# Kernel tuning notes

Measured on AMD Instinct MI355X. Metric: run time of the kernel, lower is better.

## Reference

```python
import jax, jax.numpy as jnp
import numpy as np

F = 32  # node channels (both convs)


def ecc_conv(x, src, dst, e, fgn_w, fgn_b, root, bias):
    """Edge-conditioned conv: per-edge kernel from edge feats, gather-matmul-scatter."""
    n_nodes = x.shape[0]
    n_edges = e.shape[0]
    f_in = x.shape[1]
    # filter-generating network: (E, S) -> (E, F_in*F_out) -> (E, F_in, F_out)
    kernels = (e @ fgn_w + fgn_b).reshape(n_edges, f_in, F)
    # gather source node feats, per-edge matmul
    messages = jnp.einsum('ef,efo->eo', x[src], kernels)
    # scatter-sum to target nodes
    agg = jax.ops.segment_sum(messages, dst, num_segments=n_nodes)
    return jax.nn.relu(agg + x @ root + bias)


def setup_inputs() -> dict:
    key = jax.random.key(0)
    ks = jax.random.split(key, 12)
    N, E, S = 50000, 200000, 16
    s = 0.05  # small init scale to keep activations bounded through relu
    return {
        'x': jax.random.normal(ks[0], (N, F), jnp.float32),
        'e': jax.random.normal(ks[1], (E, S), jnp.float32),
        'src': jax.random.randint(ks[2], (E,), 0, N, jnp.int32),
        'dst': jax.random.randint(ks[3], (E,), 0, N, jnp.int32),
        'fgn_w1': jax.random.normal(ks[4], (S, F * F), jnp.float32) * s,
        'fgn_b1': jnp.zeros((F * F,), jnp.float32),
        'root1': jax.random.normal(ks[5], (F, F), jnp.float32) * s,
        'bias1': jnp.zeros((F,), jnp.float32),
        'fgn_w2': jax.random.normal(ks[6], (S, F * F), jnp.float32) * s,
        'fgn_b2': jnp.zeros((F * F,), jnp.float32),
        'root2': jax.random.normal(ks[7], (F, F), jnp.float32) * s,
        'bias2': jnp.zeros((F,), jnp.float32),
        'dense_w': jax.random.normal(ks[8], (F, 1), jnp.float32) * s,
        'dense_b': jnp.zeros((1,), jnp.float32),
    }


def reference(x, e, src, dst, fgn_w1, fgn_b1, root1, bias1,
              fgn_w2, fgn_b2, root2, bias2, dense_w, dense_b):
    h = ecc_conv(x, src, dst, e, fgn_w1, fgn_b1, root1, bias1)
    h = ecc_conv(h, src, dst, e, fgn_w2, fgn_b2, root2, bias2)
    pooled = jnp.sum(h, axis=0)          # global sum pool over nodes -> (F,)
    return pooled @ dense_w + dense_b    # (1,)
```

## Files before the change

### kernel.cpp

```cpp
#include <hip/hip_runtime.h>
#include <hip/hip_bf16.h>

#define F 32
#define S 16
#define K2 544

typedef short v8s __attribute__((ext_vector_type(8)));
typedef float v4f __attribute__((ext_vector_type(4)));

__device__ __forceinline__ float bf_lo(unsigned u) { return __uint_as_float(u << 16); }
__device__ __forceinline__ float bf_hi(unsigned u) { return __uint_as_float(u & 0xffff0000u); }
__device__ __forceinline__ unsigned short f2bf(float f) {
    __hip_bfloat16 h = __float2bfloat16(f);
    return *(unsigned short*)&h;
}
__device__ __forceinline__ unsigned pack2(float a, float b) {
    return (unsigned)f2bf(a) | ((unsigned)f2bf(b) << 16);
}
static inline size_t align256(size_t b) { return (b + 255) & ~(size_t)255; }

__global__ __launch_bounds__(256) void convert_w2(
    const float* __restrict__ w1, const float* __restrict__ b1, const float* __restrict__ r1,
    const float* __restrict__ w2, const float* __restrict__ b2, const float* __restrict__ r2,
    unsigned short* __restrict__ W2t1, unsigned short* __restrict__ W2t2,
    unsigned short* __restrict__ Rt1,  unsigned short* __restrict__ Rt2)
{
    const int PER = 32 * K2 + 32 * 32;
    int tid = blockIdx.x * blockDim.x + threadIdx.x;
    if (tid >= 2 * PER) return;
    const int layer = tid / PER;
    const int rem   = tid % PER;
    const float* w = layer ? w2 : w1;
    const float* b = layer ? b2 : b1;
    const float* r = layer ? r2 : r1;
    if (rem < 32 * K2) {
        const int o = rem / K2;
        const int k = rem % K2;
        const int s = k >> 5, f = k & 31;
        const float v = (s < S) ? w[s * (F * F) + f * F + o] : b[f * F + o];
        (layer ? W2t2 : W2t1)[o * K2 + k] = f2bf(v);
    } else {
        const int q = rem - 32 * K2;
        const int o = q >> 5, f = q & 31;
        (layer ? Rt2 : Rt1)[o * F + f] = f2bf(r[f * F + o]);
    }
}

__global__ __launch_bounds__(256) void hist_kernel(
    const int* __restrict__ dst, int* __restrict__ cnt, int E)
{
    int e = blockIdx.x * blockDim.x + threadIdx.x;
    if (e < E) atomicAdd(&cnt[dst[e]], 1);
}

__global__ __launch_bounds__(256) void scan_partial(
    const int* __restrict__ cnt, int* __restrict__ partial, int N)
{
    const int i = blockIdx.x * 256 + threadIdx.x;
    int v = (i < N) ? cnt[i] : 0;
    #pragma unroll
    for (int off = 32; off > 0; off >>= 1) v += __shfl_down(v, off, 64);
    __shared__ int wsum[4];
    const int wave = threadIdx.x >> 6, lane = threadIdx.x & 63;
    if (lane == 0) wsum[wave] = v;
    __syncthreads();
    if (threadIdx.x == 0)
        partial[blockIdx.x] = wsum[0] + wsum[1] + wsum[2] + wsum[3];
}

__global__ void scan_top(int* __restrict__ partial, int M)
{
    const int t = threadIdx.x;
    int carry = 0;
    for (int base = 0; base < M; base += 64) {
        const int i = base + t;
        const int v0 = (i < M) ? partial[i] : 0;
        int v = v0;
        #pragma unroll
        for (int off = 1; off < 64; off <<= 1) {
            int u = __shfl_up(v, off, 64);
            if (t >= off) v += u;
        }
        if (i < M) partial[i] = carry + (v - v0);
        carry += __shfl(v, 63, 64);
    }
}

__global__ __launch_bounds__(256) void scan_final(
    const int* __restrict__ cnt, const int* __restrict__ partial,
    int* __restrict__ cursor, int* __restrict__ rowptr, int N)
{
    const int i = blockIdx.x * 256 + threadIdx.x;
    const int v0 = (i < N) ? cnt[i] : 0;
    int v = v0;
    const int wave = threadIdx.x >> 6, lane = threadIdx.x & 63;
    #pragma unroll
    for (int off = 1; off < 64; off <<= 1) {
        int u = __shfl_up(v, off, 64);
        if (lane >= off) v += u;
    }
    __shared__ int wsum[4];
    if (lane == 63) wsum[wave] = v;
    __syncthreads();
    int woff = 0;
    for (int ww = 0; ww < 4; ++ww) woff += (ww < wave) ? wsum[ww] : 0;
    if (i < N) {
        const int excl = partial[blockIdx.x] + woff + (v - v0);
        cursor[i] = excl;
        rowptr[i] = excl;
    }
}

__global__ __launch_bounds__(256) void scatter_kernel(
    const int* __restrict__ dst, int* __restrict__ cursor,
    int* __restrict__ perm, int E)
{
    int e = blockIdx.x * blockDim.x + threadIdx.x;
    if (e < E) {
        int p = atomicAdd(&cursor[dst[e]], 1);
        perm[p] = e;
    }
}

__global__ __launch_bounds__(256) void edge_msg(
    const float* __restrict__ xin,
    const float* __restrict__ ef,
    const int* __restrict__ src,
    const unsigned short* __restrict__ W2t,
    unsigned short* __restrict__ msg,
    int E)
{
    const int tid  = threadIdx.x;
    const int w    = tid >> 6;
    const int lane = tid & 63;
    const int lid  = lane & 15;
    const int quad = lane >> 4;

    const int tile = blockIdx.x * 4 + w;
    const int nTiles = (E + 15) >> 4;
    if (tile >= nTiles) return;

    const int  slot = tile * 16 + lid;
    const bool live = (slot < E);
    const int  e    = live ? slot : 0;
    const int  sn   = src[e];
    const float4* xp = (const float4*)(xin + (size_t)sn * F + quad * 8);
    const float4 xv0 = xp[0], xv1 = xp[1];
    const float4* efv = (const float4*)(ef + (size_t)e * S);
    const float4 c0 = efv[0], c1 = efv[1], c2 = efv[2], c3 = efv[3];

    v8s wa0[17], wa1[17];
    #pragma unroll
    for (int ck = 0; ck < 17; ++ck) {
        wa0[ck] = *(const v8s*)(W2t + (size_t)lid * K2        + ck * 32 + quad * 8);
        wa1[ck] = *(const v8s*)(W2t + (size_t)(16 + lid) * K2 + ck * 32 + quad * 8);
    }

    const float cs[S] = {c0.x, c0.y, c0.z, c0.w, c1.x, c1.y, c1.z, c1.w,
                         c2.x, c2.y, c2.z, c2.w, c3.x, c3.y, c3.z, c3.w};

    v4f acc0 = {0.f, 0.f, 0.f, 0.f};
    v4f acc1 = {0.f, 0.f, 0.f, 0.f};

    #pragma unroll
    for (int ck = 0; ck < S; ++ck) {
        const float sc = cs[ck];
        union { v8s s8; uint4 u4; } fr;
        fr.u4.x = pack2(sc * xv0.x, sc * xv0.y);
        fr.u4.y = pack2(sc * xv0.z, sc * xv0.w);
        fr.u4.z = pack2(sc * xv1.x, sc * xv1.y);
        fr.u4.w = pack2(sc * xv1.z, sc * xv1.w);
        acc0 = __builtin_amdgcn_mfma_f32_16x16x32_bf16(wa0[ck], fr.s8, acc0, 0, 0, 0);
        acc1 = __builtin_amdgcn_mfma_f32_16x16x32_bf16(wa1[ck], fr.s8, acc1, 0, 0, 0);
    }
    {
        union { v8s s8; uint4 u4; } fr;
        fr.u4.x = pack2(xv0.x, xv0.y);
        fr.u4.y = pack2(xv0.z, xv0.w);
        fr.u4.z = pack2(xv1.x, xv1.y);
        fr.u4.w = pack2(xv1.z, xv1.w);
        acc0 = __builtin_amdgcn_mfma_f32_16x16x32_bf16(wa0[16], fr.s8, acc0, 0, 0, 0);
        acc1 = __builtin_amdgcn_mfma_f32_16x16x32_bf16(wa1[16], fr.s8, acc1, 0, 0, 0);
    }

    if (live) {
        unsigned short* mp = msg + (size_t)slot * 32;
        uint2 p0, p1;
        p0.x = pack2(acc0[0], acc0[1]);
        p0.y = pack2(acc0[2], acc0[3]);
        p1.x = pack2(acc1[0], acc1[1]);
        p1.y = pack2(acc1[2], acc1[3]);
        *(uint2*)(mp + quad * 4)      = p0;
        *(uint2*)(mp + 16 + quad * 4) = p1;
    }
}

__global__ __launch_bounds__(256) void rootsum(
    const float* __restrict__ in,
    const unsigned short* __restrict__ msg,
    const int* __restrict__ perm,
    const int* __restrict__ rowptr,
    const int* __restrict__ cnt,
    const unsigned short* __restrict__ Rt,
    const float* __restrict__ bias,
    float* __restrict__ h,
    int N)
{
    __shared__ float acc[64 * 33];
    __shared__ unsigned short As[64 * F];
    const int tid  = threadIdx.x;
    const int n0   = blockIdx.x * 64;
    const int w    = tid >> 6;
    const int lane = tid & 63;
    const int lid  = lane & 15;
    const int quad = lane >> 4;

    {
        const int nl = tid >> 2;
        const int kq = tid & 3;
        int n = n0 + nl; if (n > N - 1) n = N - 1;
        const float4* xp = (const float4*)(in + (size_t)n * F + kq * 8);
        float4 v0 = xp[0], v1 = xp[1];
        uint4 pk;
        pk.x = pack2(v0.x, v0.y);
        pk.y = pack2(v0.z, v0.w);
        pk.z = pack2(v1.x, v1.y);
        pk.w = pack2(v1.z, v1.w);
        const int slot = ((nl >> 4) * 4 + kq) * 16 + (nl & 15);
        *(uint4*)(As + slot * 8) = pk;
    }

    {
        const int nl = tid >> 2;
        const int oq = tid & 3;
        const int n  = n0 + nl;
        float a[8];
        #pragma unroll
        for (int j = 0; j < 8; ++j) a[j] = 0.f;
        if (n < N) {
            const int k0 = rowptr[n];
            const int k1 = k0 + cnt[n];
            for (int k = k0; k < k1; ++k) {
                const int e = perm[k];
                const uint4 q = *(const uint4*)(msg + (size_t)e * 32 + oq * 8);
                a[0] += bf_lo(q.x); a[1] += bf_hi(q.x);
                a[2] += bf_lo(q.y); a[3] += bf_hi(q.y);
                a[4] += bf_lo(q.z); a[5] += bf_hi(q.z);
                a[6] += bf_lo(q.w); a[7] += bf_hi(q.w);
            }
        }
        float* ap = acc + nl * 33 + oq * 8;
        #pragma unroll
        for (int j = 0; j < 8; ++j) ap[j] = a[j];
    }
    __syncthreads();

    const int jt  = w & 1;
    const int ns0 = (w >> 1) * 2;
    const v8s rf = *(const v8s*)(Rt + (size_t)(jt * 16 + lid) * F + quad * 8);
    const int o0 = jt * 16 + quad * 4;
    const float4 bs = *(const float4*)(bias + o0);

    #pragma unroll
    for (int i = 0; i < 2; ++i) {
        const int ns = ns0 + i;
        const v8s af = *(const v8s*)(As + (((ns * 4 + quad) * 16) + lid) * 8);
        v4f d = {0.f, 0.f, 0.f, 0.f};
        d = __builtin_amdgcn_mfma_f32_16x16x32_bf16(rf, af, d, 0, 0, 0);
        const int n = n0 + ns * 16 + lid;
        if (n < N) {
            const float* ap = acc + (ns * 16 + lid) * 33 + o0;
            float4 hv;
            hv.x = fmaxf(d[0] + ap[0] + bs.x, 0.f);
            hv.y = fmaxf(d[1] + ap[1] + bs.y, 0.f);
            hv.z = fmaxf(d[2] + ap[2] + bs.z, 0.f);
            hv.w = fmaxf(d[3] + ap[3] + bs.w, 0.f);
            *(float4*)(h + (size_t)n * F + o0) = hv;
        }
    }
}

__global__ __launch_bounds__(256) void pool_kernel(
    const float* __restrict__ h, float* __restrict__ pooled, int N)
{
    const int c = threadIdx.x & (F - 1);
    const int rowsPerBlock = 256 / F;
    float p = 0.0f;
    for (int n = blockIdx.x * rowsPerBlock + (threadIdx.x >> 5);
         n < N; n += gridDim.x * rowsPerBlock)
        p += h[(size_t)n * F + c];
    __shared__ float red[256];
    red[threadIdx.x] = p;
    __syncthreads();
    for (int off = 128; off >= F; off >>= 1) {
        if (threadIdx.x < off) red[threadIdx.x] += red[threadIdx.x + off];
        __syncthreads();
    }
    if (threadIdx.x < F) atomicAdd(&pooled[threadIdx.x], red[threadIdx.x]);
}

__global__ void final_kernel(
    const float* __restrict__ pooled, const float* __restrict__ dw,
    const float* __restrict__ db, float* __restrict__ out)
{
    const int o = threadIdx.x;
    float v = (o < F) ? pooled[o] * dw[o] : 0.0f;
    #pragma unroll
    for (int off = 32; off > 0; off >>= 1) v += __shfl_down(v, off, 64);
    if (o == 0) out[0] = v + db[0];
}

__global__ __launch_bounds__(256, 2) void ecc_edge_slow(
    const float* __restrict__ x, const float* __restrict__ ef,
    const int* __restrict__ src, const int* __restrict__ dst,
    const float* __restrict__ W, const float* __restrict__ B,
    float* __restrict__ agg, int E)
{
    const int tid = blockIdx.x * blockDim.x + threadIdx.x;
    const bool live = (tid < E);
    const int e = live ? tid : (E - 1);
    const int sn = src[e], dn = dst[e];
    float xr[F];
    const float4* xp = (const float4*)(x + (size_t)sn * F);
    #pragma unroll
    for (int i = 0; i < F / 4; ++i) {
        float4 v = xp[i];
        xr[4*i+0] = v.x; xr[4*i+1] = v.y; xr[4*i+2] = v.z; xr[4*i+3] = v.w;
    }
    float acc[F];
    #pragma unroll
    for (int o = 0; o < F; ++o) acc[o] = 0.0f;
    const float* erow = ef + (size_t)e * S;
    for (int s = 0; s < S; ++s) {
        const float es = erow[s];
        const float* Ws = W + s * (F * F);
        #pragma unroll
        for (int f = 0; f < F; ++f) {
            const float z = es * xr[f];
            #pragma unroll
            for (int o = 0; o < F; ++o) acc[o] = fmaf(z, Ws[f * F + o], acc[o]);
        }
    }
    #pragma unroll
    for (int f = 0; f < F; ++f) {
        const float xf = xr[f];
        #pragma unroll
        for (int o = 0; o < F; ++o) acc[o] = fmaf(xf, B[f * F + o], acc[o]);
    }
    if (live) {
        float* ap = agg + (size_t)dn * F;
        #pragma unroll
        for (int o = 0; o < F; ++o) atomicAdd(ap + o, acc[o]);
    }
}

__global__ __launch_bounds__(256) void ecc_node_slow(
    const float* __restrict__ xin, const float* __restrict__ root,
    const float* __restrict__ bias, float* __restrict__ h, int N)
{
    int t = blockIdx.x * blockDim.x + threadIdx.x;
    if (t >= N * F) return;
    const int n = t >> 5, o = t & (F - 1);
    const float* xrow = xin + (size_t)n * F;
    float v = h[t] + bias[o];
    #pragma unroll
    for (int f = 0; f < F; ++f) v = fmaf(xrow[f], root[f * F + o], v);
    h[t] = fmaxf(v, 0.0f);
}

extern "C" void kernel_launch(void* const* d_in, const int* in_sizes, int n_in,
                              void* d_out, int out_size, void* d_ws, size_t ws_size,
                              hipStream_t stream) {
    const float* x      = (const float*)d_in[0];
    const float* efeat  = (const float*)d_in[1];
    const int*   src    = (const int*)d_in[2];
    const int*   dst    = (const int*)d_in[3];
    const float* fgn_w1 = (const float*)d_in[4];
    const float* fgn_b1 = (const float*)d_in[5];
    const float* root1  = (const float*)d_in[6];
    const float* bias1  = (const float*)d_in[7];
    const float* fgn_w2 = (const float*)d_in[8];
    const float* fgn_b2 = (const float*)d_in[9];
    const float* root2  = (const float*)d_in[10];
    const float* bias2  = (const float*)d_in[11];
    const float* dense_w = (const float*)d_in[12];
    const float* dense_b = (const float*)d_in[13];

    const int N = in_sizes[0] / F;
    const int E = in_sizes[2];

    const int gridP = (N + 255) / 256;

    const size_t pooledB = 256;
    const size_t cntB    = align256((size_t)N * 4);
    const size_t rowB    = align256((size_t)N * 4);
    const size_t curB    = align256((size_t)N * 4);
    const size_t partB   = align256((size_t)gridP * 4);
    const size_t permB   = align256((size_t)E * 4);
    const size_t msgB    = align256((size_t)E * 32 * 2);
    const size_t hB      = (size_t)N * F * 4;
    const size_t w2tB    = align256((size_t)32 * K2 * 2);
    const size_t rtB     = align256((size_t)32 * 32 * 2);

    const size_t offCnt  = pooledB;
    const size_t offRow  = offCnt + cntB;
    const size_t offCur  = offRow + rowB;
    const size_t offPart = offCur + curB;
    const size_t offPerm = offPart + partB;
    const size_t offMsg  = offPerm + permB;
    const size_t offH1   = offMsg + msgB;
    const size_t offH2   = offH1 + hB;
    const size_t offW1   = offH2 + hB;
    const size_t offW2   = offW1 + w2tB;
    const size_t offR1   = offW2 + w2tB;
    const size_t offR2   = offR1 + rtB;
    const size_t need    = offR2 + rtB;

    const int eB         = (E + 255) / 256;
    const int nodeBlocks = (N * F + 255) / 256;

    if (ws_size >= need) {
        float* pooled = (float*)d_ws;
        int* cnt     = (int*)((char*)d_ws + offCnt);
        int* rowptr  = (int*)((char*)d_ws + offRow);
        int* cursor  = (int*)((char*)d_ws + offCur);
        int* partial = (int*)((char*)d_ws + offPart);
        int* perm    = (int*)((char*)d_ws + offPerm);
        unsigned short* msg = (unsigned short*)((char*)d_ws + offMsg);
        float* h1    = (float*)((char*)d_ws + offH1);
        float* h2    = (float*)((char*)d_ws + offH2);
        unsigned short* W2t1 = (unsigned short*)((char*)d_ws + offW1);
        unsigned short* W2t2 = (unsigned short*)((char*)d_ws + offW2);
        unsigned short* Rt1  = (unsigned short*)((char*)d_ws + offR1);
        unsigned short* Rt2  = (unsigned short*)((char*)d_ws + offR2);

        hipMemsetAsync(d_ws, 0, pooledB + cntB, stream);

        convert_w2<<<(2 * (32 * K2 + 32 * 32) + 255) / 256, 256, 0, stream>>>(
            fgn_w1, fgn_b1, root1, fgn_w2, fgn_b2, root2, W2t1, W2t2, Rt1, Rt2);

        hist_kernel   <<<eB, 256, 0, stream>>>(dst, cnt, E);
        scan_partial  <<<gridP, 256, 0, stream>>>(cnt, partial, N);
        scan_top      <<<1, 64, 0, stream>>>(partial, gridP);
        scan_final    <<<gridP, 256, 0, stream>>>(cnt, partial, cursor, rowptr, N);
        scatter_kernel<<<eB, 256, 0, stream>>>(dst, cursor, perm, E);

        const int nTiles     = (E + 15) / 16;
        const int edgeBlocks = (nTiles + 3) / 4;
        const int rsBlocks   = (N + 63) / 64;

        edge_msg<<<edgeBlocks, 256, 0, stream>>>(x, efeat, src, W2t1, msg, E);
        rootsum <<<rsBlocks, 256, 0, stream>>>(x, msg, perm, rowptr, cnt, Rt1, bias1, h1, N);

        edge_msg<<<edgeBlocks, 256, 0, stream>>>(h1, efeat, src, W2t2, msg, E);
        rootsum <<<rsBlocks, 256, 0, stream>>>(h1, msg, perm, rowptr, cnt, Rt2, bias2, h2, N);

        pool_kernel <<<512, 256, 0, stream>>>(h2, pooled, N);
        final_kernel<<<1, 64, 0, stream>>>(pooled, dense_w, dense_b, (float*)d_out);
    } else {
        float* agg1   = (float*)d_ws;
        float* agg2   = agg1 + (size_t)N * F;
        float* pooled = agg2 + (size_t)N * F;
        hipMemsetAsync(d_ws, 0, (2 * (size_t)N * F + F) * sizeof(float), stream);
        ecc_edge_slow<<<eB, 256, 0, stream>>>(x, efeat, src, dst, fgn_w1, fgn_b1, agg1, E);
        ecc_node_slow<<<nodeBlocks, 256, 0, stream>>>(x, root1, bias1, agg1, N);
        ecc_edge_slow<<<eB, 256, 0, stream>>>(agg1, efeat, src, dst, fgn_w2, fgn_b2, agg2, E);
        ecc_node_slow<<<nodeBlocks, 256, 0, stream>>>(agg1, root2, bias2, agg2, N);
        pool_kernel <<<512, 256, 0, stream>>>(agg2, pooled, N);
        final_kernel<<<1, 64, 0, stream>>>(pooled, dense_w, dense_b, (float*)d_out);
    }
}
```

Measured before the change: 225.7 us.

## Pre-sort edges by destination and stage fragment-ordered weights in LDS

Adds a pass that permutes edge features and source indices into destination-sorted order, so edge_msg writes messages in CSR order and rootsum reads them contiguously without the perm indirection. Weights are pre-laid out in MFMA fragment order and copied once per block into shared memory, and edge_msg becomes a grid-stride loop capped at 1024 blocks, replacing per-wave global weight loads into registers. The cost is an extra gather kernel plus extra workspace for the sorted edge data, and the per-block LDS staging of the weights.

```diff
diff --git a/kernel.cpp b/kernel.cpp
--- a/kernel.cpp
+++ b/kernel.cpp
@@ -3,7 +3,6 @@
 
 #define F 32
 #define S 16
-#define K2 544
 
 typedef short v8s __attribute__((ext_vector_type(8)));
 typedef float v4f __attribute__((ext_vector_type(4)));
@@ -22,10 +21,10 @@
 __global__ __launch_bounds__(256) void convert_w2(
     const float* __restrict__ w1, const float* __restrict__ b1, const float* __restrict__ r1,
     const float* __restrict__ w2, const float* __restrict__ b2, const float* __restrict__ r2,
-    unsigned short* __restrict__ W2t1, unsigned short* __restrict__ W2t2,
-    unsigned short* __restrict__ Rt1,  unsigned short* __restrict__ Rt2)
-{
-    const int PER = 32 * K2 + 32 * 32;
+    unsigned short* __restrict__ Wf1, unsigned short* __restrict__ Wf2,
+    unsigned short* __restrict__ Rt1, unsigned short* __restrict__ Rt2)
+{
+    const int PER = 34 * 512 + 32 * 32;
     int tid = blockIdx.x * blockDim.x + threadIdx.x;
     if (tid >= 2 * PER) return;
     const int layer = tid / PER;
@@ -33,14 +32,20 @@
     const float* w = layer ? w2 : w1;
     const float* b = layer ? b2 : b1;
     const float* r = layer ? r2 : r1;
-    if (rem < 32 * K2) {
-        const int o = rem / K2;
-        const int k = rem % K2;
-        const int s = k >> 5, f = k & 31;
-        const float v = (s < S) ? w[s * (F * F) + f * F + o] : b[f * F + o];
-        (layer ? W2t2 : W2t1)[o * K2 + k] = f2bf(v);
+    if (rem < 34 * 512) {
+        const int fi   = rem >> 9;
+        const int rr   = rem & 511;
+        const int lane = rr >> 3;
+        const int j    = rr & 7;
+        const int half = fi & 1;
+        const int ck   = fi >> 1;
+        const int o    = (half << 4) | (lane & 15);
+        const int k    = ck * 32 + (lane >> 4) * 8 + j;
+        const int s    = k >> 5, f = k & 31;
+        const float v  = (s < S) ? w[s * (F * F) + f * F + o] : b[f * F + o];
+        (layer ? Wf2 : Wf1)[rem] = f2bf(v);
     } else {
-        const int q = rem - 32 * K2;
+        const int q = rem - 34 * 512;
         const int o = q >> 5, f = q & 31;
         (layer ? Rt2 : Rt1)[o * F + f] = f2bf(r[f * F + o]);
     }
@@ -122,83 +127,99 @@
     }
 }
 
+__global__ __launch_bounds__(256) void esort_kernel(
+    const float* __restrict__ ef, const int* __restrict__ src,
+    const int* __restrict__ perm,
+    float* __restrict__ ef_s, int* __restrict__ src_s, int E)
+{
+    const int gid = blockIdx.x * blockDim.x + threadIdx.x;
+    const int slot = gid >> 2;
+    if (slot >= E) return;
+    const int q = gid & 3;
+    const int e = perm[slot];
+    ((float4*)(ef_s + (size_t)slot * S))[q] = ((const float4*)(ef + (size_t)e * S))[q];
+    if (q == 0) src_s[slot] = src[e];
+}
+
 __global__ __launch_bounds__(256) void edge_msg(
     const float* __restrict__ xin,
-    const float* __restrict__ ef,
-    const int* __restrict__ src,
-    const unsigned short* __restrict__ W2t,
+    const float* __restrict__ ef_s,
+    const int* __restrict__ src_s,
+    const unsigned short* __restrict__ Wf,
     unsigned short* __restrict__ msg,
     int E)
 {
+    __shared__ v8s Wl[34 * 64];
     const int tid  = threadIdx.x;
     const int w    = tid >> 6;
     const int lane = tid & 63;
     const int lid  = lane & 15;
     const int quad = lane >> 4;
 
-    const int tile = blockIdx.x * 4 + w;
+    {
+        const uint4* s = (const uint4*)Wf;
+        uint4* d = (uint4*)Wl;
+        #pragma unroll
+        for (int i = 0; i < 9; ++i) {
+            const int idx = tid + 256 * i;
+            if (idx < 2176) d[idx] = s[idx];
+        }
+    }
+    __syncthreads();
+
     const int nTiles = (E + 15) >> 4;
-    if (tile >= nTiles) return;
-
-    const int  slot = tile * 16 + lid;
-    const bool live = (slot < E);
-    const int  e    = live ? slot : 0;
-    const int  sn   = src[e];
-    const float4* xp = (const float4*)(xin + (size_t)sn * F + quad * 8);
-    const float4 xv0 = xp[0], xv1 = xp[1];
-    const float4* efv = (const float4*)(ef + (size_t)e * S);
-    const float4 c0 = efv[0], c1 = efv[1], c2 = efv[2], c3 = efv[3];
-
-    v8s wa0[17], wa1[17];
-    #pragma unroll
-    for (int ck = 0; ck < 17; ++ck) {
-        wa0[ck] = *(const v8s*)(W2t + (size_t)lid * K2        + ck * 32 + quad * 8);
-        wa1[ck] = *(const v8s*)(W2t + (size_t)(16 + lid) * K2 + ck * 32 + quad * 8);
-    }
-
-    const float cs[S] = {c0.x, c0.y, c0.z, c0.w, c1.x, c1.y, c1.z, c1.w,
-                         c2.x, c2.y, c2.z, c2.w, c3.x, c3.y, c3.z, c3.w};
-
-    v4f acc0 = {0.f, 0.f, 0.f, 0.f};
-    v4f acc1 = {0.f, 0.f, 0.f, 0.f};
-
-    #pragma unroll
-    for (int ck = 0; ck < S; ++ck) {
-        const float sc = cs[ck];
-        union { v8s s8; uint4 u4; } fr;
-        fr.u4.x = pack2(sc * xv0.x, sc * xv0.y);
-        fr.u4.y = pack2(sc * xv0.z, sc * xv0.w);
-        fr.u4.z = pack2(sc * xv1.x, sc * xv1.y);
-        fr.u4.w = pack2(sc * xv1.z, sc * xv1.w);
-        acc0 = __builtin_amdgcn_mfma_f32_16x16x32_bf16(wa0[ck], fr.s8, acc0, 0, 0, 0);
-        acc1 = __builtin_amdgcn_mfma_f32_16x16x32_bf16(wa1[ck], fr.s8, acc1, 0, 0, 0);
-    }
-    {
-        union { v8s s8; uint4 u4; } fr;
-        fr.u4.x = pack2(xv0.x, xv0.y);
-        fr.u4.y = pack2(xv0.z, xv0.w);
-        fr.u4.z = pack2(xv1.x, xv1.y);
-        fr.u4.w = pack2(xv1.z, xv1.w);
-        acc0 = __builtin_amdgcn_mfma_f32_16x16x32_bf16(wa0[16], fr.s8, acc0, 0, 0, 0);
-        acc1 = __builtin_amdgcn_mfma_f32_16x16x32_bf16(wa1[16], fr.s8, acc1, 0, 0, 0);
-    }
-
-    if (live) {
-        unsigned short* mp = msg + (size_t)slot * 32;
-        uint2 p0, p1;
-        p0.x = pack2(acc0[0], acc0[1]);
-        p0.y = pack2(acc0[2], acc0[3]);
-        p1.x = pack2(acc1[0], acc1[1]);
-        p1.y = pack2(acc1[2], acc1[3]);
-        *(uint2*)(mp + quad * 4)      = p0;
-        *(uint2*)(mp + 16 + quad * 4) = p1;
+    for (int tile = blockIdx.x * 4 + w; tile < nTiles; tile += gridDim.x * 4) {
+        const int  slot = tile * 16 + lid;
+        const bool live = (slot < E);
+        const int  s    = live ? slot : 0;
+        const int  sn   = src_s[s];
+        const float4* xp = (const float4*)(xin + (size_t)sn * F + quad * 8);
+        const float4 xv0 = xp[0], xv1 = xp[1];
+        const float4* efv = (const float4*)(ef_s + (size_t)s * S);
+        const float4 c0 = efv[0], c1 = efv[1], c2 = efv[2], c3 = efv[3];
+        const float cs[S] = {c0.x, c0.y, c0.z, c0.w, c1.x, c1.y, c1.z, c1.w,
+                             c2.x, c2.y, c2.z, c2.w, c3.x, c3.y, c3.z, c3.w};
+
+        v4f acc0 = {0.f, 0.f, 0.f, 0.f};
+        v4f acc1 = {0.f, 0.f, 0.f, 0.f};
+
+        #pragma unroll
+        for (int ck = 0; ck < S; ++ck) {
+            const float sc = cs[ck];
+            union { v8s s8; uint4 u4; } fr;
+            fr.u4.x = pack2(sc * xv0.x, sc * xv0.y);
+            fr.u4.y = pack2(sc * xv0.z, sc * xv0.w);
+            fr.u4.z = pack2(sc * xv1.x, sc * xv1.y);
+            fr.u4.w = pack2(sc * xv1.z, sc * xv1.w);
+            acc0 = __builtin_amdgcn_mfma_f32_16x16x32_bf16(Wl[(2 * ck) * 64 + lane],     fr.s8, acc0, 0, 0, 0);
+            acc1 = __builtin_amdgcn_mfma_f32_16x16x32_bf16(Wl[(2 * ck + 1) * 64 + lane], fr.s8, acc1, 0, 0, 0);
+        }
+        {
+            union { v8s s8; uint4 u4; } fr;
+            fr.u4.x = pack2(xv0.x, xv0.y);
+            fr.u4.y = pack2(xv0.z, xv0.w);
+            fr.u4.z = pack2(xv1.x, xv1.y);
+            fr.u4.w = pack2(xv1.z, xv1.w);
+            acc0 = __builtin_amdgcn_mfma_f32_16x16x32_bf16(Wl[32 * 64 + lane], fr.s8, acc0, 0, 0, 0);
+            acc1 = __builtin_amdgcn_mfma_f32_16x16x32_bf16(Wl[33 * 64 + lane], fr.s8, acc1, 0, 0, 0);
+        }
+
+        if (live) {
+            unsigned short* mp = msg + (size_t)slot * 32;
+            uint2 p0, p1;
+            p0.x = pack2(acc0[0], acc0[1]);
+            p0.y = pack2(acc0[2], acc0[3]);
+            p1.x = pack2(acc1[0], acc1[1]);
+            p1.y = pack2(acc1[2], acc1[3]);
+            *(uint2*)(mp + quad * 4)      = p0;
+            *(uint2*)(mp + 16 + quad * 4) = p1;
+        }
     }
 }
 
 __global__ __launch_bounds__(256) void rootsum(
     const float* __restrict__ in,
     const unsigned short* __restrict__ msg,
-    const int* __restrict__ perm,
     const int* __restrict__ rowptr,
     const int* __restrict__ cnt,
     const unsigned short* __restrict__ Rt,
@@ -241,8 +262,7 @@
             const int k0 = rowptr[n];
             const int k1 = k0 + cnt[n];
             for (int k = k0; k < k1; ++k) {
-                const int e = perm[k];
-                const uint4 q = *(const uint4*)(msg + (size_t)e * 32 + oq * 8);
+                const uint4 q = *(const uint4*)(msg + (size_t)k * 32 + oq * 8);
                 a[0] += bf_lo(q.x); a[1] += bf_hi(q.x);
                 a[2] += bf_lo(q.y); a[3] += bf_hi(q.y);
                 a[4] += bf_lo(q.z); a[5] += bf_hi(q.z);
@@ -397,9 +417,11 @@
     const size_t curB    = align256((size_t)N * 4);
     const size_t partB   = align256((size_t)gridP * 4);
     const size_t permB   = align256((size_t)E * 4);
+    const size_t efsB    = align256((size_t)E * S * 4);
+    const size_t srcsB   = align256((size_t)E * 4);
     const size_t msgB    = align256((size_t)E * 32 * 2);
     const size_t hB      = (size_t)N * F * 4;
-    const size_t w2tB    = align256((size_t)32 * K2 * 2);
+    const size_t wfB     = align256((size_t)34 * 512 * 2);
     const size_t rtB     = align256((size_t)32 * 32 * 2);
 
     const size_t offCnt  = pooledB;
@@ -407,12 +429,14 @@
     const size_t offCur  = offRow + rowB;
     const size_t offPart = offCur + curB;
     const size_t offPerm = offPart + partB;
-    const size_t offMsg  = offPerm + permB;
+    const size_t offEfs  = offPerm + permB;
+    const size_t offSrcs = offEfs + efsB;
+    const size_t offMsg  = offSrcs + srcsB;
     const size_t offH1   = offMsg + msgB;
     const size_t offH2   = offH1 + hB;
     const size_t offW1   = offH2 + hB;
-    const size_t offW2   = offW1 + w2tB;
-    const size_t offR1   = offW2 + w2tB;
+    const size_t offW2   = offW1 + wfB;
+    const size_t offR1   = offW2 + wfB;
     const size_t offR2   = offR1 + rtB;
     const size_t need    = offR2 + rtB;
 
@@ -426,34 +450,38 @@
         int* cursor  = (int*)((char*)d_ws + offCur);
         int* partial = (int*)((char*)d_ws + offPart);
         int* perm    = (int*)((char*)d_ws + offPerm);
+        float* ef_s  = (float*)((char*)d_ws + offEfs);
+        int*   src_s = (int*)((char*)d_ws + offSrcs);
         unsigned short* msg = (unsigned short*)((char*)d_ws + offMsg);
         float* h1    = (float*)((char*)d_ws + offH1);
         float* h2    = (float*)((char*)d_ws + offH2);
-        unsigned short* W2t1 = (unsigned short*)((char*)d_ws + offW1);
-        unsigned short* W2t2 = (unsigned short*)((char*)d_ws + offW2);
-        unsigned short* Rt1  = (unsigned short*)((char*)d_ws + offR1);
-        unsigned short* Rt2  = (unsigned short*)((char*)d_ws + offR2);
+        unsigned short* Wf1 = (unsigned short*)((char*)d_ws + offW1);
+        unsigned short* Wf2 = (unsigned short*)((char*)d_ws + offW2);
+        unsigned short* Rt1 = (unsigned short*)((char*)d_ws + offR1);
+        unsigned short* Rt2 = (unsigned short*)((char*)d_ws + offR2);
 
         hipMemsetAsync(d_ws, 0, pooledB + cntB, stream);
 
-        convert_w2<<<(2 * (32 * K2 + 32 * 32) + 255) / 256, 256, 0, stream>>>(
-            fgn_w1, fgn_b1, root1, fgn_w2, fgn_b2, root2, W2t1, W2t2, Rt1, Rt2);
+        convert_w2<<<(2 * 18432 + 255) / 256, 256, 0, stream>>>(
+            fgn_w1, fgn_b1, root1, fgn_w2, fgn_b2, root2, Wf1, Wf2, Rt1, Rt2);
 
         hist_kernel   <<<eB, 256, 0, stream>>>(dst, cnt, E);
         scan_partial  <<<gridP, 256, 0, stream>>>(cnt, partial, N);
         scan_top      <<<1, 64, 0, stream>>>(partial, gridP);
         scan_final    <<<gridP, 256, 0, stream>>>(cnt, partial, cursor, rowptr, N);
         scatter_kernel<<<eB, 256, 0, stream>>>(dst, cursor, perm, E);
+        esort_kernel  <<<(E * 4 + 255) / 256, 256, 0, stream>>>(efeat, src, perm, ef_s, src_s, E);
 
         const int nTiles     = (E + 15) / 16;
-        const int edgeBlocks = (nTiles + 3) / 4;
+        int edgeBlocks = (nTiles + 3) / 4;
+        if (edgeBlocks > 1024) edgeBlocks = 1024;
         const int rsBlocks   = (N + 63) / 64;
 
-        edge_msg<<<edgeBlocks, 256, 0, stream>>>(x, efeat, src, W2t1, msg, E);
-        rootsum <<<rsBlocks, 256, 0, stream>>>(x, msg, perm, rowptr, cnt, Rt1, bias1, h1, N);
-
-        edge_msg<<<edgeBlocks, 256, 0, stream>>>(h1, efeat, src, W2t2, msg, E);
-        rootsum <<<rsBlocks, 256, 0, stream>>>(h1, msg, perm, rowptr, cnt, Rt2, bias2, h2, N);
+        edge_msg<<<edgeBlocks, 256, 0, stream>>>(x, ef_s, src_s, Wf1, msg, E);
+        rootsum <<<rsBlocks, 256, 0, stream>>>(x, msg, rowptr, cnt, Rt1, bias1, h1, N);
+
+        edge_msg<<<edgeBlocks, 256, 0, stream>>>(h1, ef_s, src_s, Wf2, msg, E);
+        rootsum <<<rsBlocks, 256, 0, stream>>>(h1, msg, rowptr, cnt, Rt2, bias2, h2, N);
 
         pool_kernel <<<512, 256, 0, stream>>>(h2, pooled, N);
         final_kernel<<<1, 64, 0, stream>>>(pooled, dense_w, dense_b, (float*)d_out);
```

After: 203.0 us. 1.11x faster.
